# Optimization experiments

Hardware: AMD Instinct MI355X
Metric: run time of the kernel (lower is better)

The kernel has to match this reference:

```python
import jax, jax.numpy as jnp
import numpy as np


def setup_inputs() -> dict:
    key = jax.random.key(0)
    k1, k2, k3 = jax.random.split(key, 3)
    B, N, F, D = 8, 2048, 512, 512
    x = jax.random.normal(k1, (B, N, F), dtype=jnp.float32)
    a = jax.random.uniform(k2, (B, N, N), dtype=jnp.float32)
    kernel = jax.random.normal(k3, (F, D), dtype=jnp.float32) * (1.0 / np.sqrt(F))
    return {"x": x, "a": a, "kernel": kernel}


def reference(x, a, kernel):
    # t = a @ x : [B,N,N] x [B,N,F] -> [B,N,F]
    t = jnp.einsum('bnm,bmf->bnf', a, x)
    # feature transform: [B,N,F] x [F,D] -> [B,N,D]
    out = jnp.einsum('bnf,fd->bnd', t, kernel)
    # dropout is inference-mode (identity); no bias
    out = jax.nn.relu(out)
    # padded mask: zero rows of x produce zero outputs
    mask = (jnp.sum((x != 0).astype(jnp.float32), axis=-1, keepdims=True) > 0).astype(jnp.float32)
    return out * mask
```

## Files before the change

kernel.cpp:

```cpp
#include <hip/hip_runtime.h>

typedef __bf16 bf16x8 __attribute__((ext_vector_type(8)));
typedef float f32x4 __attribute__((ext_vector_type(4)));
typedef unsigned int u32x4 __attribute__((ext_vector_type(4)));

__device__ __forceinline__ unsigned short f2bf(float f) {
  unsigned u = __builtin_bit_cast(unsigned, f);
  u += 0x7FFFu + ((u >> 16) & 1u);
  return (unsigned short)(u >> 16);
}

__device__ __forceinline__ void gl2lds16(const void* g, void* l) {
  __builtin_amdgcn_global_load_lds((const __attribute__((address_space(1))) void*)g,
                                   (__attribute__((address_space(3))) void*)l, 16, 0, 0);
}

__device__ __forceinline__ bf16x8 cvt8v(f32x4 a, f32x4 b) {
  bf16x8 r;
  r[0] = (__bf16)a[0]; r[1] = (__bf16)a[1]; r[2] = (__bf16)a[2]; r[3] = (__bf16)a[3];
  r[4] = (__bf16)b[0]; r[5] = (__bf16)b[1]; r[6] = (__bf16)b[2]; r[7] = (__bf16)b[3];
  return r;
}

__global__ void transpose_cvt(const float* __restrict__ in, unsigned short* __restrict__ out) {
  __shared__ float tile[32][33];
  const int r0 = blockIdx.x * 32, c0 = blockIdx.y * 32;
  const int tx = threadIdx.x, ty = threadIdx.y;
#pragma unroll
  for (int i = 0; i < 4; ++i) tile[ty + i * 8][tx] = in[(size_t)(r0 + ty + i * 8) * 512 + c0 + tx];
  __syncthreads();
#pragma unroll
  for (int i = 0; i < 4; ++i) {
    const int cc = ty + i * 8;
    out[(size_t)(c0 + cc) * 512 + r0 + tx] = f2bf(tile[tx][cc]);
  }
}

template <int APITCH, int BPITCH, int NT, bool IS_Y>
__global__ __launch_bounds__(512, 1) void gemm8p(const float* __restrict__ A0,
                                                 const unsigned short* __restrict__ B0,
                                                 unsigned short* __restrict__ yT,
                                                 int* __restrict__ mask,
                                                 float* __restrict__ out) {
  __shared__ __align__(16) char lds[131072];

  const int bid = blockIdx.x;
  int b, m0, n0;
  const float* Ab;
  const unsigned short* Bb;
  if constexpr (IS_Y) {
    const int mt = bid >> 1, nt = bid & 1;
    b = mt >> 4; m0 = (mt & 15) * 128; n0 = nt * 256;
    Ab = A0 + ((size_t)b * 2048 + m0) * APITCH;
    Bb = B0 + (size_t)n0 * BPITCH;
  } else {
    b = bid & 7;
    const int idx = bid >> 3;
    m0 = (idx & 15) * 128; n0 = (idx >> 4) * 256;
    Ab = A0 + ((size_t)b * 2048 + m0) * APITCH;
    Bb = B0 + ((size_t)b * 512 + n0) * BPITCH;
  }

  const int tid = threadIdx.x, w = tid >> 6, L = tid & 63;
  const int wr = w >> 2, wc = w & 3, r = L & 15, hi = L >> 4;

  const char* aSrc = (const char*)(Ab + (size_t)(w * 16 + r) * APITCH + hi * 4);
  const char* bSrc0 = (const char*)(Bb + (size_t)(w * 32 + r) * BPITCH + hi * 8);
  const char* bSrc1 = (const char*)(Bb + (size_t)(w * 32 + 16 + r) * BPITCH + hi * 8);

  int aro[4], bro[4];
#pragma unroll
  for (int mi = 0; mi < 4; ++mi)
    aro[mi] = (((wr * 4 + mi) * 2 + (hi >> 1)) << 10) + ((hi & 1) << 9) + r * 16;
#pragma unroll
  for (int ni = 0; ni < 4; ++ni) bro[ni] = 16384 + ((wc * 4 + ni) << 10) + L * 16;

  f32x4 acc[4][4] = {};
  unsigned anz[4] = {0u, 0u, 0u, 0u};

#define STAGE(SLOT, TA)                                                          \
  {                                                                              \
    char* ls = lds + (SLOT) * 32768;                                             \
    gl2lds16(aSrc + (size_t)(TA) * 128, ls + ((w * 2 + 0) << 10));               \
    gl2lds16(aSrc + (size_t)(TA) * 128 + 64, ls + ((w * 2 + 1) << 10));          \
    gl2lds16(bSrc0 + (size_t)(TA) * 64, ls + 16384 + ((w * 2 + 0) << 10));       \
    gl2lds16(bSrc1 + (size_t)(TA) * 64, ls + 16384 + ((w * 2 + 1) << 10));       \
  }

#define ORBITS(mi, lo, hh)                                                       \
  if constexpr (IS_Y) {                                                          \
    if (wc == 0) {                                                               \
      u32x4 u0 = __builtin_bit_cast(u32x4, lo), u1 = __builtin_bit_cast(u32x4, hh); \
      anz[mi] |= (u0[0] | u0[1] | u0[2] | u0[3] | u1[0] | u1[1] | u1[2] | u1[3]) & \
                 0x7fffffffu;                                                    \
    }                                                                            \
  }

  STAGE(0, 0)
  STAGE(1, 1)
  STAGE(2, 2)
  asm volatile("s_waitcnt vmcnt(8)" ::: "memory");
  __builtin_amdgcn_sched_barrier(0);
  __builtin_amdgcn_s_barrier();
  __builtin_amdgcn_sched_barrier(0);

#pragma unroll 1
  for (int t = 0; t < NT; ++t) {
    const int slot = (t + 3) & 3, cur = t & 3;
    const int ta = (t + 3 < NT) ? (t + 3) : (NT - 1);
    STAGE(slot, ta)
    __builtin_amdgcn_sched_barrier(0);
    const char* cb = lds + cur * 32768;

    bf16x8 bfr[4];
#pragma unroll
    for (int ni = 0; ni < 4; ++ni) bfr[ni] = *(const bf16x8*)(cb + bro[ni]);
    f32x4 lo0 = *(const f32x4*)(cb + aro[0]), hh0 = *(const f32x4*)(cb + aro[0] + 256);
    f32x4 lo1 = *(const f32x4*)(cb + aro[1]), hh1 = *(const f32x4*)(cb + aro[1] + 256);
    asm volatile("s_waitcnt lgkmcnt(0)" ::: "memory");
    __builtin_amdgcn_sched_barrier(0);
    ORBITS(0, lo0, hh0)
    ORBITS(1, lo1, hh1)
    bf16x8 af0 = cvt8v(lo0, hh0), af1 = cvt8v(lo1, hh1);
    __builtin_amdgcn_s_setprio(1);
#pragma unroll
    for (int ni = 0; ni < 4; ++ni)
      acc[0][ni] = __builtin_amdgcn_mfma_f32_16x16x32_bf16(af0, bfr[ni], acc[0][ni], 0, 0, 0);
#pragma unroll
    for (int ni = 0; ni < 4; ++ni)
      acc[1][ni] = __builtin_amdgcn_mfma_f32_16x16x32_bf16(af1, bfr[ni], acc[1][ni], 0, 0, 0);
    __builtin_amdgcn_s_setprio(0);

    f32x4 lo2 = *(const f32x4*)(cb + aro[2]), hh2 = *(const f32x4*)(cb + aro[2] + 256);
    f32x4 lo3 = *(const f32x4*)(cb + aro[3]), hh3 = *(const f32x4*)(cb + aro[3] + 256);
    asm volatile("s_waitcnt lgkmcnt(0)" ::: "memory");
    __builtin_amdgcn_sched_barrier(0);
    ORBITS(2, lo2, hh2)
    ORBITS(3, lo3, hh3)
    bf16x8 af2 = cvt8v(lo2, hh2), af3 = cvt8v(lo3, hh3);
    __builtin_amdgcn_s_setprio(1);
#pragma unroll
    for (int ni = 0; ni < 4; ++ni)
      acc[2][ni] = __builtin_amdgcn_mfma_f32_16x16x32_bf16(af2, bfr[ni], acc[2][ni], 0, 0, 0);
#pragma unroll
    for (int ni = 0; ni < 4; ++ni)
      acc[3][ni] = __builtin_amdgcn_mfma_f32_16x16x32_bf16(af3, bfr[ni], acc[3][ni], 0, 0, 0);
    __builtin_amdgcn_s_setprio(0);

    asm volatile("s_waitcnt vmcnt(8)" ::: "memory");
    __builtin_amdgcn_sched_barrier(0);
    __builtin_amdgcn_s_barrier();
    __builtin_amdgcn_sched_barrier(0);
  }
  asm volatile("s_waitcnt vmcnt(0)" ::: "memory");

#undef STAGE
#undef ORBITS

  if constexpr (IS_Y) {
    if (wc == 0) {
#pragma unroll
      for (int mi = 0; mi < 4; ++mi) {
        unsigned v = anz[mi];
        v |= __shfl_xor(v, 16);
        v |= __shfl_xor(v, 32);
        if (hi == 0) mask[b * 2048 + m0 + wr * 64 + mi * 16 + r] = (v != 0u) ? 1 : 0;
      }
    }
#pragma unroll
    for (int mi = 0; mi < 4; ++mi)
#pragma unroll
      for (int ni = 0; ni < 4; ++ni) {
        const int col = n0 + wc * 64 + ni * 16 + r;
        const int nrow = m0 + wr * 64 + mi * 16 + hi * 4;
        ushort4 s;
        s.x = f2bf(acc[mi][ni][0]);
        s.y = f2bf(acc[mi][ni][1]);
        s.z = f2bf(acc[mi][ni][2]);
        s.w = f2bf(acc[mi][ni][3]);
        *(ushort4*)(yT + (((size_t)b * 512 + col) << 11) + nrow) = s;
      }
  } else {
    const int* mrow = mask + b * 2048 + m0 + wr * 64;
#pragma unroll
    for (int mi = 0; mi < 4; ++mi) {
      const int4 mv = *(const int4*)(mrow + mi * 16 + hi * 4);
      const int mvv[4] = {mv.x, mv.y, mv.z, mv.w};
#pragma unroll
      for (int ni = 0; ni < 4; ++ni) {
        const int col = n0 + wc * 64 + ni * 16 + r;
        float* op = out + (size_t)(b * 2048 + m0 + wr * 64 + mi * 16 + hi * 4) * 512 + col;
#pragma unroll
        for (int rr = 0; rr < 4; ++rr) {
          float v = fmaxf(acc[mi][ni][rr], 0.0f);
          if (mvv[rr] == 0) v = 0.0f;
          op[(size_t)rr * 512] = v;
        }
      }
    }
  }
}

extern "C" void kernel_launch(void* const* d_in, const int* in_sizes, int n_in,
                              void* d_out, int out_size, void* d_ws, size_t ws_size,
                              hipStream_t stream) {
  const float* x = (const float*)d_in[0];
  const float* a = (const float*)d_in[1];
  const float* wk = (const float*)d_in[2];
  float* out = (float*)d_out;

  char* ws = (char*)d_ws;
  unsigned short* wT = (unsigned short*)ws;
  unsigned short* yT = (unsigned short*)(ws + (1u << 19));
  int* mask = (int*)(ws + (1u << 19) + (16u << 20));

  transpose_cvt<<<dim3(16, 16), dim3(32, 8), 0, stream>>>(wk, wT);
  gemm8p<512, 512, 16, true><<<256, 512, 0, stream>>>(x, wT, yT, mask, nullptr);
  gemm8p<2048, 2048, 64, false><<<256, 512, 0, stream>>>(a, yT, nullptr, mask, out);
}
```

Measured before the change: 99.50 us.

## Retile big A·Y GEMM to 64x512 blocks so the fp32 adjacency is read once

The second GEMM (adjacency times transformed features) is split into its own kernel. Each block now covers 64 rows by all 512 output columns instead of 128x256, so every fp32 row of the large adjacency matrix is loaded by only one block rather than two. It moves from a 4-stage to a 3-stage LDS pipeline with larger per-stage B tiles. The trade-off is that each block re-reads the full bf16 Y slice, each wave holds 2x8 accumulators, and there is less latency-hiding depth.

New measurement: 113.4 us. +14.0%, slower.

```diff
diff --git a/kernel.cpp b/kernel.cpp
--- a/kernel.cpp
+++ b/kernel.cpp
@@ -36,30 +36,17 @@
   }
 }
 
-template <int APITCH, int BPITCH, int NT, bool IS_Y>
-__global__ __launch_bounds__(512, 1) void gemm8p(const float* __restrict__ A0,
+__global__ __launch_bounds__(512, 1) void gemm_y(const float* __restrict__ A0,
                                                  const unsigned short* __restrict__ B0,
                                                  unsigned short* __restrict__ yT,
-                                                 int* __restrict__ mask,
-                                                 float* __restrict__ out) {
+                                                 int* __restrict__ mask) {
+  constexpr int APITCH = 512, BPITCH = 512, NT = 16;
   __shared__ __align__(16) char lds[131072];
-
   const int bid = blockIdx.x;
-  int b, m0, n0;
-  const float* Ab;
-  const unsigned short* Bb;
-  if constexpr (IS_Y) {
-    const int mt = bid >> 1, nt = bid & 1;
-    b = mt >> 4; m0 = (mt & 15) * 128; n0 = nt * 256;
-    Ab = A0 + ((size_t)b * 2048 + m0) * APITCH;
-    Bb = B0 + (size_t)n0 * BPITCH;
-  } else {
-    b = bid & 7;
-    const int idx = bid >> 3;
-    m0 = (idx & 15) * 128; n0 = (idx >> 4) * 256;
-    Ab = A0 + ((size_t)b * 2048 + m0) * APITCH;
-    Bb = B0 + ((size_t)b * 512 + n0) * BPITCH;
-  }
+  const int mt = bid >> 1, nt = bid & 1;
+  const int b = mt >> 4, m0 = (mt & 15) * 128, n0 = nt * 256;
+  const float* Ab = A0 + ((size_t)b * 2048 + m0) * APITCH;
+  const unsigned short* Bb = B0 + (size_t)n0 * BPITCH;
 
   const int tid = threadIdx.x, w = tid >> 6, L = tid & 63;
   const int wr = w >> 2, wc = w & 3, r = L & 15, hi = L >> 4;
@@ -87,15 +74,6 @@
     gl2lds16(bSrc1 + (size_t)(TA) * 64, ls + 16384 + ((w * 2 + 1) << 10));       \
   }
 
-#define ORBITS(mi, lo, hh)                                                       \
-  if constexpr (IS_Y) {                                                          \
-    if (wc == 0) {                                                               \
-      u32x4 u0 = __builtin_bit_cast(u32x4, lo), u1 = __builtin_bit_cast(u32x4, hh); \
-      anz[mi] |= (u0[0] | u0[1] | u0[2] | u0[3] | u1[0] | u1[1] | u1[2] | u1[3]) & \
-                 0x7fffffffu;                                                    \
-    }                                                                            \
-  }
-
   STAGE(0, 0)
   STAGE(1, 1)
   STAGE(2, 2)
@@ -119,8 +97,12 @@
     f32x4 lo1 = *(const f32x4*)(cb + aro[1]), hh1 = *(const f32x4*)(cb + aro[1] + 256);
     asm volatile("s_waitcnt lgkmcnt(0)" ::: "memory");
     __builtin_amdgcn_sched_barrier(0);
-    ORBITS(0, lo0, hh0)
-    ORBITS(1, lo1, hh1)
+    if (wc == 0) {
+      u32x4 u0 = __builtin_bit_cast(u32x4, lo0), u1 = __builtin_bit_cast(u32x4, hh0);
+      anz[0] |= (u0[0] | u0[1] | u0[2] | u0[3] | u1[0] | u1[1] | u1[2] | u1[3]) & 0x7fffffffu;
+      u32x4 v0 = __builtin_bit_cast(u32x4, lo1), v1 = __builtin_bit_cast(u32x4, hh1);
+      anz[1] |= (v0[0] | v0[1] | v0[2] | v0[3] | v1[0] | v1[1] | v1[2] | v1[3]) & 0x7fffffffu;
+    }
     bf16x8 af0 = cvt8v(lo0, hh0), af1 = cvt8v(lo1, hh1);
     __builtin_amdgcn_s_setprio(1);
 #pragma unroll
@@ -135,8 +117,12 @@
     f32x4 lo3 = *(const f32x4*)(cb + aro[3]), hh3 = *(const f32x4*)(cb + aro[3] + 256);
     asm volatile("s_waitcnt lgkmcnt(0)" ::: "memory");
     __builtin_amdgcn_sched_barrier(0);
-    ORBITS(2, lo2, hh2)
-    ORBITS(3, lo3, hh3)
+    if (wc == 0) {
+      u32x4 u0 = __builtin_bit_cast(u32x4, lo2), u1 = __builtin_bit_cast(u32x4, hh2);
+      anz[2] |= (u0[0] | u0[1] | u0[2] | u0[3] | u1[0] | u1[1] | u1[2] | u1[3]) & 0x7fffffffu;
+      u32x4 v0 = __builtin_bit_cast(u32x4, lo3), v1 = __builtin_bit_cast(u32x4, hh3);
+      anz[3] |= (v0[0] | v0[1] | v0[2] | v0[3] | v1[0] | v1[1] | v1[2] | v1[3]) & 0x7fffffffu;
+    }
     bf16x8 af2 = cvt8v(lo2, hh2), af3 = cvt8v(lo3, hh3);
     __builtin_amdgcn_s_setprio(1);
 #pragma unroll
@@ -153,49 +139,128 @@
     __builtin_amdgcn_sched_barrier(0);
   }
   asm volatile("s_waitcnt vmcnt(0)" ::: "memory");
-
 #undef STAGE
-#undef ORBITS
-
-  if constexpr (IS_Y) {
-    if (wc == 0) {
-#pragma unroll
-      for (int mi = 0; mi < 4; ++mi) {
-        unsigned v = anz[mi];
-        v |= __shfl_xor(v, 16);
-        v |= __shfl_xor(v, 32);
-        if (hi == 0) mask[b * 2048 + m0 + wr * 64 + mi * 16 + r] = (v != 0u) ? 1 : 0;
-      }
-    }
-#pragma unroll
-    for (int mi = 0; mi < 4; ++mi)
-#pragma unroll
-      for (int ni = 0; ni < 4; ++ni) {
-        const int col = n0 + wc * 64 + ni * 16 + r;
-        const int nrow = m0 + wr * 64 + mi * 16 + hi * 4;
-        ushort4 s;
-        s.x = f2bf(acc[mi][ni][0]);
-        s.y = f2bf(acc[mi][ni][1]);
-        s.z = f2bf(acc[mi][ni][2]);
-        s.w = f2bf(acc[mi][ni][3]);
-        *(ushort4*)(yT + (((size_t)b * 512 + col) << 11) + nrow) = s;
-      }
-  } else {
-    const int* mrow = mask + b * 2048 + m0 + wr * 64;
+
+  if (wc == 0) {
 #pragma unroll
     for (int mi = 0; mi < 4; ++mi) {
-      const int4 mv = *(const int4*)(mrow + mi * 16 + hi * 4);
-      const int mvv[4] = {mv.x, mv.y, mv.z, mv.w};
-#pragma unroll
-      for (int ni = 0; ni < 4; ++ni) {
-        const int col = n0 + wc * 64 + ni * 16 + r;
-        float* op = out + (size_t)(b * 2048 + m0 + wr * 64 + mi * 16 + hi * 4) * 512 + col;
-#pragma unroll
-        for (int rr = 0; rr < 4; ++rr) {
-          float v = fmaxf(acc[mi][ni][rr], 0.0f);
-          if (mvv[rr] == 0) v = 0.0f;
-          op[(size_t)rr * 512] = v;
-        }
+      unsigned v = anz[mi];
+      v |= __shfl_xor(v, 16);
+      v |= __shfl_xor(v, 32);
+      if (hi == 0) mask[b * 2048 + m0 + wr * 64 + mi * 16 + r] = (v != 0u) ? 1 : 0;
+    }
+  }
+#pragma unroll
+  for (int mi = 0; mi < 4; ++mi)
+#pragma unroll
+    for (int ni = 0; ni < 4; ++ni) {
+      const int col = n0 + wc * 64 + ni * 16 + r;
+      const int nrow = m0 + wr * 64 + mi * 16 + hi * 4;
+      ushort4 s;
+      s.x = f2bf(acc[mi][ni][0]);
+      s.y = f2bf(acc[mi][ni][1]);
+      s.z = f2bf(acc[mi][ni][2]);
+      s.w = f2bf(acc[mi][ni][3]);
+      *(ushort4*)(yT + (((size_t)b * 512 + col) << 11) + nrow) = s;
+    }
+}
+
+template <int APITCH, int BPITCH, int NT>
+__global__ __launch_bounds__(512, 1) void gemm_big2(const float* __restrict__ A0,
+                                                    const unsigned short* __restrict__ B0,
+                                                    const int* __restrict__ mask,
+                                                    float* __restrict__ out) {
+  __shared__ __align__(16) char lds[122880];
+
+  const int bid = blockIdx.x;
+  const int b = bid & 7, mt = bid >> 3;
+  const int m0 = mt * 64;
+  const float* Ab = A0 + ((size_t)b * 2048 + m0) * APITCH;
+  const unsigned short* Bb = B0 + (size_t)b * 512 * BPITCH;
+
+  const int tid = threadIdx.x, w = tid >> 6, L = tid & 63;
+  const int wr = w >> 2, wc = w & 3, r = L & 15, hi = L >> 4;
+
+  const char* aSrc =
+      (const char*)(Ab + (size_t)((w >> 1) * 16 + r) * APITCH) + (w & 1) * 64 + hi * 16;
+
+  const char* bSrc[4];
+#pragma unroll
+  for (int j = 0; j < 4; ++j)
+    bSrc[j] = (const char*)(Bb + (size_t)((w * 4 + j) * 16 + r) * BPITCH) + hi * 16;
+
+  int aro[2];
+#pragma unroll
+  for (int mi = 0; mi < 2; ++mi)
+    aro[mi] = (((wr * 2 + mi) * 2 + (hi >> 1)) << 10) + ((hi & 1) << 9) + r * 16;
+  int bro[8];
+#pragma unroll
+  for (int ni = 0; ni < 8; ++ni) bro[ni] = 8192 + ((wc * 8 + ni) << 10) + L * 16;
+
+  f32x4 acc[2][8] = {};
+
+#define STAGE(SLOT, TA)                                                       \
+  {                                                                           \
+    char* ls = lds + (SLOT) * 40960;                                          \
+    gl2lds16(aSrc + (size_t)(TA) * 128, ls + (w << 10));                      \
+    _Pragma("unroll") for (int j = 0; j < 4; ++j)                             \
+        gl2lds16(bSrc[j] + (size_t)(TA) * 64, ls + 8192 + ((w * 4 + j) << 10)); \
+  }
+
+  STAGE(0, 0)
+  STAGE(1, 1)
+  asm volatile("s_waitcnt vmcnt(5)" ::: "memory");
+  __builtin_amdgcn_sched_barrier(0);
+  __builtin_amdgcn_s_barrier();
+  __builtin_amdgcn_sched_barrier(0);
+
+#pragma unroll 1
+  for (int t = 0; t < NT; ++t) {
+    const int slot = (t + 2) % 3;
+    const int ta = (t + 2 < NT) ? (t + 2) : (NT - 1);
+    STAGE(slot, ta)
+    __builtin_amdgcn_sched_barrier(0);
+
+    const char* cb = lds + (t % 3) * 40960;
+    bf16x8 bfr[8];
+#pragma unroll
+    for (int ni = 0; ni < 8; ++ni) bfr[ni] = *(const bf16x8*)(cb + bro[ni]);
+    f32x4 lo0 = *(const f32x4*)(cb + aro[0]), hh0 = *(const f32x4*)(cb + aro[0] + 256);
+    f32x4 lo1 = *(const f32x4*)(cb + aro[1]), hh1 = *(const f32x4*)(cb + aro[1] + 256);
+    asm volatile("s_waitcnt lgkmcnt(0)" ::: "memory");
+    __builtin_amdgcn_sched_barrier(0);
+    bf16x8 af0 = cvt8v(lo0, hh0), af1 = cvt8v(lo1, hh1);
+    __builtin_amdgcn_s_setprio(1);
+#pragma unroll
+    for (int ni = 0; ni < 8; ++ni)
+      acc[0][ni] = __builtin_amdgcn_mfma_f32_16x16x32_bf16(af0, bfr[ni], acc[0][ni], 0, 0, 0);
+#pragma unroll
+    for (int ni = 0; ni < 8; ++ni)
+      acc[1][ni] = __builtin_amdgcn_mfma_f32_16x16x32_bf16(af1, bfr[ni], acc[1][ni], 0, 0, 0);
+    __builtin_amdgcn_s_setprio(0);
+
+    asm volatile("s_waitcnt vmcnt(5)" ::: "memory");
+    __builtin_amdgcn_sched_barrier(0);
+    __builtin_amdgcn_s_barrier();
+    __builtin_amdgcn_sched_barrier(0);
+  }
+  asm volatile("s_waitcnt vmcnt(0)" ::: "memory");
+#undef STAGE
+
+  const int* mrow = mask + b * 2048 + m0 + wr * 32;
+#pragma unroll
+  for (int mi = 0; mi < 2; ++mi) {
+    const int4 mv = *(const int4*)(mrow + mi * 16 + hi * 4);
+    const int mvv[4] = {mv.x, mv.y, mv.z, mv.w};
+#pragma unroll
+    for (int ni = 0; ni < 8; ++ni) {
+      const int col = wc * 128 + ni * 16 + r;
+      float* op = out + (size_t)(b * 2048 + m0 + wr * 32 + mi * 16 + hi * 4) * 512 + col;
+#pragma unroll
+      for (int rr = 0; rr < 4; ++rr) {
+        float v = fmaxf(acc[mi][ni][rr], 0.0f);
+        if (mvv[rr] == 0) v = 0.0f;
+        op[(size_t)rr * 512] = v;
       }
     }
   }
@@ -215,6 +280,6 @@
   int* mask = (int*)(ws + (1u << 19) + (16u << 20));
 
   transpose_cvt<<<dim3(16, 16), dim3(32, 8), 0, stream>>>(wk, wT);
-  gemm8p<512, 512, 16, true><<<256, 512, 0, stream>>>(x, wT, yT, mask, nullptr);
-  gemm8p<2048, 2048, 64, false><<<256, 512, 0, stream>>>(a, yT, nullptr, mask, out);
-}
+  gemm_y<<<256, 512, 0, stream>>>(x, wT, yT, mask);
+  gemm_big2<2048, 2048, 64><<<256, 512, 0, stream>>>(a, yT, mask, out);
+}
```

## Restructure the large GEMM: convert A to bf16 once in LDS, stream B through registers

Applied to the files above, without the earlier changes.

Splits the templated GEMM into a dedicated kernel for the x·W stage and a new kernel for the large a·y product. In the new kernel, fp32 A tiles are loaded into registers, converted to bf16 once per block and written to a swizzled, double-buffered LDS tile. B fragments are read straight from global memory into registers, with the K step per iteration doubled to 64. This removes the redundant per-wave fp32-to-bf16 conversion and the large fp32 LDS staging. In exchange the prefetch is now a single register stage instead of a deeper async LDS pipeline, and B loads are duplicated across wave rows, so memory latency may be less well hidden.

Measured after the change: 122.5 us. 1.23x slower.

```diff
diff --git a/kernel.cpp b/kernel.cpp
--- a/kernel.cpp
+++ b/kernel.cpp
@@ -36,30 +36,17 @@
   }
 }
 
-template <int APITCH, int BPITCH, int NT, bool IS_Y>
-__global__ __launch_bounds__(512, 1) void gemm8p(const float* __restrict__ A0,
+__global__ __launch_bounds__(512, 1) void gemm_y(const float* __restrict__ A0,
                                                  const unsigned short* __restrict__ B0,
                                                  unsigned short* __restrict__ yT,
-                                                 int* __restrict__ mask,
-                                                 float* __restrict__ out) {
+                                                 int* __restrict__ mask) {
+  constexpr int APITCH = 512, BPITCH = 512, NT = 16;
   __shared__ __align__(16) char lds[131072];
-
   const int bid = blockIdx.x;
-  int b, m0, n0;
-  const float* Ab;
-  const unsigned short* Bb;
-  if constexpr (IS_Y) {
-    const int mt = bid >> 1, nt = bid & 1;
-    b = mt >> 4; m0 = (mt & 15) * 128; n0 = nt * 256;
-    Ab = A0 + ((size_t)b * 2048 + m0) * APITCH;
-    Bb = B0 + (size_t)n0 * BPITCH;
-  } else {
-    b = bid & 7;
-    const int idx = bid >> 3;
-    m0 = (idx & 15) * 128; n0 = (idx >> 4) * 256;
-    Ab = A0 + ((size_t)b * 2048 + m0) * APITCH;
-    Bb = B0 + ((size_t)b * 512 + n0) * BPITCH;
-  }
+  const int mt = bid >> 1, nt = bid & 1;
+  const int b = mt >> 4, m0 = (mt & 15) * 128, n0 = nt * 256;
+  const float* Ab = A0 + ((size_t)b * 2048 + m0) * APITCH;
+  const unsigned short* Bb = B0 + (size_t)n0 * BPITCH;
 
   const int tid = threadIdx.x, w = tid >> 6, L = tid & 63;
   const int wr = w >> 2, wc = w & 3, r = L & 15, hi = L >> 4;
@@ -87,15 +74,6 @@
     gl2lds16(bSrc1 + (size_t)(TA) * 64, ls + 16384 + ((w * 2 + 1) << 10));       \
   }
 
-#define ORBITS(mi, lo, hh)                                                       \
-  if constexpr (IS_Y) {                                                          \
-    if (wc == 0) {                                                               \
-      u32x4 u0 = __builtin_bit_cast(u32x4, lo), u1 = __builtin_bit_cast(u32x4, hh); \
-      anz[mi] |= (u0[0] | u0[1] | u0[2] | u0[3] | u1[0] | u1[1] | u1[2] | u1[3]) & \
-                 0x7fffffffu;                                                    \
-    }                                                                            \
-  }
-
   STAGE(0, 0)
   STAGE(1, 1)
   STAGE(2, 2)
@@ -119,8 +97,12 @@
     f32x4 lo1 = *(const f32x4*)(cb + aro[1]), hh1 = *(const f32x4*)(cb + aro[1] + 256);
     asm volatile("s_waitcnt lgkmcnt(0)" ::: "memory");
     __builtin_amdgcn_sched_barrier(0);
-    ORBITS(0, lo0, hh0)
-    ORBITS(1, lo1, hh1)
+    if (wc == 0) {
+      u32x4 u0 = __builtin_bit_cast(u32x4, lo0), u1 = __builtin_bit_cast(u32x4, hh0);
+      anz[0] |= (u0[0] | u0[1] | u0[2] | u0[3] | u1[0] | u1[1] | u1[2] | u1[3]) & 0x7fffffffu;
+      u32x4 v0 = __builtin_bit_cast(u32x4, lo1), v1 = __builtin_bit_cast(u32x4, hh1);
+      anz[1] |= (v0[0] | v0[1] | v0[2] | v0[3] | v1[0] | v1[1] | v1[2] | v1[3]) & 0x7fffffffu;
+    }
     bf16x8 af0 = cvt8v(lo0, hh0), af1 = cvt8v(lo1, hh1);
     __builtin_amdgcn_s_setprio(1);
 #pragma unroll
@@ -135,8 +117,12 @@
     f32x4 lo3 = *(const f32x4*)(cb + aro[3]), hh3 = *(const f32x4*)(cb + aro[3] + 256);
     asm volatile("s_waitcnt lgkmcnt(0)" ::: "memory");
     __builtin_amdgcn_sched_barrier(0);
-    ORBITS(2, lo2, hh2)
-    ORBITS(3, lo3, hh3)
+    if (wc == 0) {
+      u32x4 u0 = __builtin_bit_cast(u32x4, lo2), u1 = __builtin_bit_cast(u32x4, hh2);
+      anz[2] |= (u0[0] | u0[1] | u0[2] | u0[3] | u1[0] | u1[1] | u1[2] | u1[3]) & 0x7fffffffu;
+      u32x4 v0 = __builtin_bit_cast(u32x4, lo3), v1 = __builtin_bit_cast(u32x4, hh3);
+      anz[3] |= (v0[0] | v0[1] | v0[2] | v0[3] | v1[0] | v1[1] | v1[2] | v1[3]) & 0x7fffffffu;
+    }
     bf16x8 af2 = cvt8v(lo2, hh2), af3 = cvt8v(lo3, hh3);
     __builtin_amdgcn_s_setprio(1);
 #pragma unroll
@@ -153,49 +139,132 @@
     __builtin_amdgcn_sched_barrier(0);
   }
   asm volatile("s_waitcnt vmcnt(0)" ::: "memory");
-
 #undef STAGE
-#undef ORBITS
-
-  if constexpr (IS_Y) {
-    if (wc == 0) {
-#pragma unroll
-      for (int mi = 0; mi < 4; ++mi) {
-        unsigned v = anz[mi];
-        v |= __shfl_xor(v, 16);
-        v |= __shfl_xor(v, 32);
-        if (hi == 0) mask[b * 2048 + m0 + wr * 64 + mi * 16 + r] = (v != 0u) ? 1 : 0;
-      }
-    }
-#pragma unroll
-    for (int mi = 0; mi < 4; ++mi)
-#pragma unroll
-      for (int ni = 0; ni < 4; ++ni) {
-        const int col = n0 + wc * 64 + ni * 16 + r;
-        const int nrow = m0 + wr * 64 + mi * 16 + hi * 4;
-        ushort4 s;
-        s.x = f2bf(acc[mi][ni][0]);
-        s.y = f2bf(acc[mi][ni][1]);
-        s.z = f2bf(acc[mi][ni][2]);
-        s.w = f2bf(acc[mi][ni][3]);
-        *(ushort4*)(yT + (((size_t)b * 512 + col) << 11) + nrow) = s;
-      }
-  } else {
-    const int* mrow = mask + b * 2048 + m0 + wr * 64;
+
+  if (wc == 0) {
 #pragma unroll
     for (int mi = 0; mi < 4; ++mi) {
-      const int4 mv = *(const int4*)(mrow + mi * 16 + hi * 4);
-      const int mvv[4] = {mv.x, mv.y, mv.z, mv.w};
-#pragma unroll
-      for (int ni = 0; ni < 4; ++ni) {
-        const int col = n0 + wc * 64 + ni * 16 + r;
-        float* op = out + (size_t)(b * 2048 + m0 + wr * 64 + mi * 16 + hi * 4) * 512 + col;
-#pragma unroll
-        for (int rr = 0; rr < 4; ++rr) {
-          float v = fmaxf(acc[mi][ni][rr], 0.0f);
-          if (mvv[rr] == 0) v = 0.0f;
-          op[(size_t)rr * 512] = v;
-        }
+      unsigned v = anz[mi];
+      v |= __shfl_xor(v, 16);
+      v |= __shfl_xor(v, 32);
+      if (hi == 0) mask[b * 2048 + m0 + wr * 64 + mi * 16 + r] = (v != 0u) ? 1 : 0;
+    }
+  }
+#pragma unroll
+  for (int mi = 0; mi < 4; ++mi)
+#pragma unroll
+    for (int ni = 0; ni < 4; ++ni) {
+      const int col = n0 + wc * 64 + ni * 16 + r;
+      const int nrow = m0 + wr * 64 + mi * 16 + hi * 4;
+      ushort4 s;
+      s.x = f2bf(acc[mi][ni][0]);
+      s.y = f2bf(acc[mi][ni][1]);
+      s.z = f2bf(acc[mi][ni][2]);
+      s.w = f2bf(acc[mi][ni][3]);
+      *(ushort4*)(yT + (((size_t)b * 512 + col) << 11) + nrow) = s;
+    }
+}
+
+template <int NT>
+__global__ __launch_bounds__(512, 1) void gemm_bigr(const float* __restrict__ a,
+                                                    const unsigned short* __restrict__ yT,
+                                                    const int* __restrict__ mask,
+                                                    float* __restrict__ out) {
+  __shared__ __align__(16) char Abuf[2][16384];
+
+  const int bid = blockIdx.x;
+  const int b = bid & 7, idx = bid >> 3;
+  const int m0 = (idx & 15) * 128, n0 = (idx >> 4) * 256;
+  const float* Ab = a + ((size_t)b * 2048 + m0) * 2048;
+  const unsigned short* Bb = yT + ((size_t)b * 512 + n0) * 2048;
+
+  const int tid = threadIdx.x, w = tid >> 6, L = tid & 63;
+  const int wr = w >> 2, wc = w & 3, r = L & 15, hi = L >> 4;
+
+  const int arow = tid >> 2, ac4 = tid & 3;
+  const float* ap = Ab + (size_t)arow * 2048 + ac4 * 16;
+  const int aw0 = arow * 128 + (((ac4 * 2 + 0) ^ (arow & 7)) << 4);
+  const int aw1 = arow * 128 + (((ac4 * 2 + 1) ^ (arow & 7)) << 4);
+
+  int aoff[4][2];
+#pragma unroll
+  for (int mi = 0; mi < 4; ++mi)
+#pragma unroll
+    for (int kk = 0; kk < 2; ++kk)
+      aoff[mi][kk] = ((wr * 64 + mi * 16 + r) * 128 + kk * 64 + hi * 16) ^ ((r & 7) << 4);
+
+  const unsigned short* bp[4];
+#pragma unroll
+  for (int ni = 0; ni < 4; ++ni)
+    bp[ni] = Bb + (size_t)(wc * 64 + ni * 16 + r) * 2048 + hi * 8;
+
+  f32x4 acc[4][4] = {};
+  bf16x8 bc0[4][2], bc1[4][2];
+  f32x4 q0, q1, q2, q3;
+
+#pragma unroll
+  for (int ni = 0; ni < 4; ++ni)
+#pragma unroll
+    for (int kk = 0; kk < 2; ++kk) bc0[ni][kk] = *(const bf16x8*)(bp[ni] + kk * 32);
+  q0 = *(const f32x4*)(ap);
+  q1 = *(const f32x4*)(ap + 4);
+  q2 = *(const f32x4*)(ap + 8);
+  q3 = *(const f32x4*)(ap + 12);
+  *(bf16x8*)(&Abuf[0][aw0]) = cvt8v(q0, q1);
+  *(bf16x8*)(&Abuf[0][aw1]) = cvt8v(q2, q3);
+  __syncthreads();
+
+#define BIG_BODY(TT, BUF, BCC, BCN)                                             \
+  {                                                                             \
+    const int tn = (TT) + 1;                                                    \
+    const bool more = (tn < NT);                                                \
+    if (more) {                                                                 \
+      _Pragma("unroll") for (int ni = 0; ni < 4; ++ni)                          \
+          _Pragma("unroll") for (int kk = 0; kk < 2; ++kk)                      \
+              BCN[ni][kk] = *(const bf16x8*)(bp[ni] + tn * 64 + kk * 32);       \
+      const float* apn = ap + tn * 64;                                          \
+      q0 = *(const f32x4*)(apn);                                                \
+      q1 = *(const f32x4*)(apn + 4);                                            \
+      q2 = *(const f32x4*)(apn + 8);                                            \
+      q3 = *(const f32x4*)(apn + 12);                                           \
+    }                                                                           \
+    bf16x8 af[4][2];                                                            \
+    _Pragma("unroll") for (int mi = 0; mi < 4; ++mi)                            \
+        _Pragma("unroll") for (int kk = 0; kk < 2; ++kk)                        \
+            af[mi][kk] = *(const bf16x8*)(&Abuf[BUF][aoff[mi][kk]]);            \
+    _Pragma("unroll") for (int kk = 0; kk < 2; ++kk)                            \
+        _Pragma("unroll") for (int mi = 0; mi < 4; ++mi)                        \
+            _Pragma("unroll") for (int ni = 0; ni < 4; ++ni)                    \
+                acc[mi][ni] = __builtin_amdgcn_mfma_f32_16x16x32_bf16(          \
+                    af[mi][kk], BCC[ni][kk], acc[mi][ni], 0, 0, 0);             \
+    if (more) {                                                                 \
+      *(bf16x8*)(&Abuf[(BUF) ^ 1][aw0]) = cvt8v(q0, q1);                        \
+      *(bf16x8*)(&Abuf[(BUF) ^ 1][aw1]) = cvt8v(q2, q3);                        \
+      __syncthreads();                                                          \
+    }                                                                           \
+  }
+
+#pragma unroll 1
+  for (int t = 0; t < NT; t += 2) {
+    BIG_BODY(t, 0, bc0, bc1)
+    BIG_BODY(t + 1, 1, bc1, bc0)
+  }
+#undef BIG_BODY
+
+  const int* mrow = mask + b * 2048 + m0 + wr * 64;
+#pragma unroll
+  for (int mi = 0; mi < 4; ++mi) {
+    const int4 mv = *(const int4*)(mrow + mi * 16 + hi * 4);
+    const int mvv[4] = {mv.x, mv.y, mv.z, mv.w};
+#pragma unroll
+    for (int ni = 0; ni < 4; ++ni) {
+      const int col = n0 + wc * 64 + ni * 16 + r;
+      float* op = out + (size_t)(b * 2048 + m0 + wr * 64 + mi * 16 + hi * 4) * 512 + col;
+#pragma unroll
+      for (int rr = 0; rr < 4; ++rr) {
+        float v = fmaxf(acc[mi][ni][rr], 0.0f);
+        if (mvv[rr] == 0) v = 0.0f;
+        op[(size_t)rr * 512] = v;
       }
     }
   }
@@ -215,6 +284,6 @@
   int* mask = (int*)(ws + (1u << 19) + (16u << 20));
 
   transpose_cvt<<<dim3(16, 16), dim3(32, 8), 0, stream>>>(wk, wT);
-  gemm8p<512, 512, 16, true><<<256, 512, 0, stream>>>(x, wT, yT, mask, nullptr);
-  gemm8p<2048, 2048, 64, false><<<256, 512, 0, stream>>>(a, yT, nullptr, mask, out);
-}
+  gemm_y<<<256, 512, 0, stream>>>(x, wT, yT, mask);
+  gemm_bigr<32><<<256, 512, 0, stream>>>(a, yT, mask, out);
+}
```
